# Kernel tuning notes

Hardware: AMD Instinct MI355X
Metric: run time of the kernel (lower is better)

The kernel has to match this reference:

```python
import jax, jax.numpy as jnp
import numpy as np

D = 1024
H = 16
B = 4
S = 2048
NEG = -1000000000.0


def setup_inputs() -> dict:
    key = jax.random.key(0)
    ks = jax.random.split(key, 12)
    s = 0.02
    inp = {
        "Q": jax.random.normal(ks[0], (B, S, D), jnp.float32),
        "K": jax.random.normal(ks[1], (B, S, D), jnp.float32),
        "V": jax.random.normal(ks[2], (B, S, D), jnp.float32),
        # causal mask, broadcastable to [B, H, S, S]
        "mask": jnp.broadcast_to(jnp.tril(jnp.ones((S, S), bool)), (B, 1, S, S)),
        "Wq": jax.random.normal(ks[3], (D, D), jnp.float32) * s,
        "bq": jnp.zeros((D,), jnp.float32),
        "Wk": jax.random.normal(ks[4], (D, D), jnp.float32) * s,
        "bk": jnp.zeros((D,), jnp.float32),
        "Wv": jax.random.normal(ks[5], (D, D), jnp.float32) * s,
        "bv": jnp.zeros((D,), jnp.float32),
        "Wo": jax.random.normal(ks[6], (D, D), jnp.float32) * s,
        "bo": jnp.zeros((D,), jnp.float32),
    }
    return inp


def reference(Q, K, V, mask, Wq, bq, Wk, bk, Wv, bv, Wo, bo):
    d = D // H  # head dim
    def split(x):  # [B,S,D] -> [B,H,S,d]
        Bx, Sx, _ = x.shape
        return x.reshape(Bx, Sx, H, d).transpose(0, 2, 1, 3)

    q = split(Q @ Wq + bq)
    k = split(K @ Wk + bk)
    v = split(V @ Wv + bv)

    scores = jnp.einsum("bhsd,bhtd->bhst", q, k) / jnp.sqrt(jnp.float32(d))
    scores = jnp.where(mask, scores, NEG)
    attn = jax.nn.softmax(scores, axis=-1)
    out = jnp.einsum("bhst,bhtd->bhsd", attn, v)  # [B,H,S,d]
    out = out.transpose(0, 2, 1, 3).reshape(Q.shape[0], Q.shape[1], D)
    return out @ Wo + bo
```

## Files before the change

kernel.cpp:

```cpp
#include <hip/hip_runtime.h>
#include <hip/hip_bf16.h>
#include <type_traits>

#define DEV __device__ __forceinline__

typedef short bf16x8 __attribute__((ext_vector_type(8)));
typedef float f32x4 __attribute__((ext_vector_type(4)));
typedef float f32x16 __attribute__((ext_vector_type(16)));
typedef unsigned u32x4 __attribute__((ext_vector_type(4)));

static DEV unsigned short f2bf(float f) {
  unsigned u = __builtin_bit_cast(unsigned, f);
  u += 0x7FFFu + ((u >> 16) & 1u);
  return (unsigned short)(u >> 16);
}

static DEV unsigned cvtpk(float lo, float hi) {
  unsigned d;
  asm("v_cvt_pk_bf16_f32 %0, %1, %2" : "=v"(d) : "v"(lo), "v"(hi));
  return d;
}

static DEV void pl32(unsigned& x, unsigned& y) {
  asm("v_permlane32_swap_b32 %0, %1" : "+v"(x), "+v"(y));
}

static DEV void gl_lds16(const void* g, void* l) {
  __builtin_amdgcn_global_load_lds(
      (const __attribute__((address_space(1))) unsigned*)g,
      (__attribute__((address_space(3))) unsigned*)l, 16, 0, 0);
}

#define QSCALE 0.18033688f

__global__ __launch_bounds__(256) void wtrans4(const float* __restrict__ W0,
                                               const float* __restrict__ W1,
                                               const float* __restrict__ W2,
                                               const float* __restrict__ W3,
                                               unsigned short* __restrict__ T0,
                                               unsigned short* __restrict__ T1,
                                               unsigned short* __restrict__ T2,
                                               unsigned short* __restrict__ T3) {
  const int z = blockIdx.z;
  const float* W = z == 0 ? W0 : z == 1 ? W1 : z == 2 ? W2 : W3;
  unsigned short* Wt = z == 0 ? T0 : z == 1 ? T1 : z == 2 ? T2 : T3;
  const float wsc = (z == 0) ? QSCALE : 1.0f;
  __shared__ __align__(16) unsigned short T[64][72];
  const int tid = threadIdx.x;
  const int k0 = blockIdx.x * 64, n0 = blockIdx.y * 64;
  const int r = tid >> 4, c4 = (tid & 15) * 4;
  for (int j = 0; j < 4; ++j) {
    int row = j * 16 + r;
    float4 v = *(const float4*)&W[(size_t)(k0 + row) * 1024 + n0 + c4];
    ushort4 w;
    w.x = f2bf(v.x * wsc); w.y = f2bf(v.y * wsc);
    w.z = f2bf(v.z * wsc); w.w = f2bf(v.w * wsc);
    *(ushort4*)&T[row][c4] = w;
  }
  __syncthreads();
  for (int j = 0; j < 4; ++j) {
    int n = j * 16 + r;
    ushort4 w;
    w.x = T[c4 + 0][n]; w.y = T[c4 + 1][n]; w.z = T[c4 + 2][n]; w.w = T[c4 + 3][n];
    *(ushort4*)&Wt[(size_t)(n0 + n) * 1024 + k0 + c4] = w;
  }
}

template <typename InT, typename OutT, bool TRANSV>
DEV void gemm_lds_body(unsigned short* SMG, const InT* __restrict__ X,
                       const unsigned short* __restrict__ Wt,
                       const float* __restrict__ bias, OutT* __restrict__ Y,
                       float bsc) {
  constexpr bool AF32 = std::is_same_v<InT, float>;
  constexpr int HBUF = 24576;
  const int tid = threadIdx.x, lane = tid & 63, wid = tid >> 6;
  const int id = blockIdx.y * 32 + blockIdx.x;
  const int xcd = id & 7, jj = id >> 3;
  const int m0 = (xcd * 4 + (jj & 3)) * 256;
  const int n0 = (jj >> 2) * 128;
  const int wm = (wid >> 1) * 64, wn = (wid & 1) * 64;
  f32x4 acc[4][4] = {};

  const int srowA = tid >> 3;
  const int slotA = ((tid & 7) ^ (srowA & 7)) * 8;
  const int rB = wid * 16 + (lane >> 3);
  const int scolB = (((lane & 7) ^ ((lane >> 3) & 7))) * 8;
  const unsigned short* gB = &Wt[(size_t)(n0 + rB) * 1024 + scolB];
  const unsigned short* gAb = nullptr;
  const float* gAf = nullptr;
  float4 aF[8];

#define ABUF(P) (SMG + (P)*HBUF)
#define BBUF(P) (SMG + (P)*HBUF + 16384)
#define DSWRITE_A(P)                                                              \
  do {                                                                            \
    _Pragma("unroll") for (int q = 0; q < 4; ++q) {                               \
      uint4 w;                                                                    \
      w.x = cvtpk(aF[2 * q].x, aF[2 * q].y);                                      \
      w.y = cvtpk(aF[2 * q].z, aF[2 * q].w);                                      \
      w.z = cvtpk(aF[2 * q + 1].x, aF[2 * q + 1].y);                              \
      w.w = cvtpk(aF[2 * q + 1].z, aF[2 * q + 1].w);                              \
      *(uint4*)&ABUF(P)[(srowA + q * 64) * 64 + slotA] = w;                       \
    }                                                                             \
  } while (0)
#define LOAD_AF(K0)                                                               \
  do {                                                                            \
    _Pragma("unroll") for (int q = 0; q < 4; ++q) {                               \
      aF[2 * q] = *(const float4*)(gAf + (size_t)q * 65536 + (K0));               \
      aF[2 * q + 1] = *(const float4*)(gAf + (size_t)q * 65536 + (K0) + 4);       \
    }                                                                             \
  } while (0)
#define STAGE_B(P, K0)                                                            \
  do {                                                                            \
    _Pragma("unroll") for (int q = 0; q < 2; ++q)                                 \
        gl_lds16(gB + (size_t)q * 8 * 1024 + (K0),                                \
                 &BBUF(P)[(wid * 16 + q * 8) * 64]);                              \
  } while (0)
#define STAGE_AB16(P, K0)                                                         \
  do {                                                                            \
    _Pragma("unroll") for (int q = 0; q < 4; ++q)                                 \
        gl_lds16(gAb + (size_t)q * 8 * 1024 + (K0),                               \
                 &ABUF(P)[(wid * 32 + q * 8) * 64]);                              \
  } while (0)

  if constexpr (AF32) {
    gAf = &X[(size_t)(m0 + srowA) * 1024 + (tid & 7) * 8];
    LOAD_AF(0);
    DSWRITE_A(0);
    LOAD_AF(64);
  } else {
    gAb = &X[(size_t)(m0 + wid * 32 + (lane >> 3)) * 1024 + scolB];
    STAGE_AB16(0, 0);
  }
  STAGE_B(0, 0);
  __syncthreads();

  for (int t = 0; t < 16; ++t) {
    const int p = t & 1;
    if (t + 1 < 16) {
      const int kn = (t + 1) * 64;
      STAGE_B(p ^ 1, kn);
      if constexpr (AF32) {
        DSWRITE_A(p ^ 1);
      } else {
        STAGE_AB16(p ^ 1, kn);
      }
    }
    __builtin_amdgcn_sched_barrier(0);
    if constexpr (AF32) {
      if (t + 2 < 16) LOAD_AF((t + 2) * 64);
    }
    const unsigned short* Asp = ABUF(p);
    const unsigned short* Bsp = BBUF(p);
#pragma unroll
    for (int kk = 0; kk < 2; ++kk) {
      const int kb = ((kk * 4 + (lane >> 4)) ^ (lane & 7)) * 8;
      bf16x8 af[4], bfr[4];
#pragma unroll
      for (int i = 0; i < 4; ++i)
        af[i] = *(const bf16x8*)&Asp[(wm + i * 16 + (lane & 15)) * 64 + kb];
#pragma unroll
      for (int i = 0; i < 4; ++i)
        bfr[i] = *(const bf16x8*)&Bsp[(wn + i * 16 + (lane & 15)) * 64 + kb];
      __builtin_amdgcn_s_setprio(1);
#pragma unroll
      for (int mi = 0; mi < 4; ++mi)
#pragma unroll
        for (int ni = 0; ni < 4; ++ni)
          acc[mi][ni] =
              __builtin_amdgcn_mfma_f32_16x16x32_bf16(af[mi], bfr[ni], acc[mi][ni], 0, 0, 0);
      __builtin_amdgcn_s_setprio(0);
    }
    __syncthreads();
  }
#undef LOAD_AF
#undef DSWRITE_A
#undef STAGE_B
#undef STAGE_AB16
#undef ABUF
#undef BBUF

  if constexpr (TRANSV) {
    const int bt = m0 >> 11;
    const int s0 = m0 & 2047;
    const int h0 = n0 >> 6;
    unsigned short* Tl = SMG;
#pragma unroll
    for (int cch = 0; cch < 4; ++cch) {
      __syncthreads();
      if ((wid >> 1) == cch) {
#pragma unroll
        for (int ni = 0; ni < 4; ++ni) {
          const int n = wn + ni * 16 + (lane & 15);
          const float bv = bias[n0 + n] * bsc;
#pragma unroll
          for (int mi = 0; mi < 4; ++mi) {
            const int mloc = mi * 16 + (lane >> 4) * 4;
#pragma unroll
            for (int r = 0; r < 4; r += 2) {
              const unsigned pk = cvtpk(acc[mi][ni][r] + bv, acc[mi][ni][r + 1] + bv);
              *(unsigned*)&Tl[n * 72 + mloc + r] = pk;
            }
          }
        }
      }
      __syncthreads();
      const int m8 = (tid & 7) * 8;
#pragma unroll
      for (int it = 0; it < 2; ++it) {
        const int nr = (tid >> 3) + it * 64;
        const int h = h0 + (nr >> 6), dv = nr & 63;
        uint4 v = *(const uint4*)&Tl[nr * 72 + m8];
        *(uint4*)&((unsigned short*)Y)[(((size_t)bt * 16 + h) * 64 + dv) * 2048 +
                                       s0 + cch * 64 + m8] = v;
      }
    }
  } else {
    for (int ni = 0; ni < 4; ++ni) {
      const int col = n0 + wn + ni * 16 + (lane & 15);
      const float bv = bias[col] * bsc;
      for (int mi = 0; mi < 4; ++mi) {
        const int row = m0 + wm + mi * 16 + (lane >> 4) * 4;
        for (int r = 0; r < 4; ++r) {
          float v = acc[mi][ni][r] + bv;
          if constexpr (std::is_same_v<OutT, float>)
            Y[(size_t)(row + r) * 1024 + col] = v;
          else
            Y[(size_t)(row + r) * 1024 + col] = f2bf(v);
        }
      }
    }
  }
}

__global__ __launch_bounds__(512) void gemm_qkv3(
    const float* __restrict__ X0, const float* __restrict__ X1,
    const float* __restrict__ X2, const unsigned short* __restrict__ W0,
    const unsigned short* __restrict__ W1, const unsigned short* __restrict__ W2,
    const float* __restrict__ b0, const float* __restrict__ b1,
    const float* __restrict__ b2, unsigned short* __restrict__ Y0,
    unsigned short* __restrict__ Y1, unsigned short* __restrict__ Y2) {
  __shared__ __align__(16) unsigned short SMG[49152];
  const int z = blockIdx.z;
  const float* X = z == 0 ? X0 : z == 1 ? X1 : X2;
  const unsigned short* Wt = z == 0 ? W0 : z == 1 ? W1 : W2;
  const float* bias = z == 0 ? b0 : z == 1 ? b1 : b2;
  unsigned short* Y = z == 0 ? Y0 : z == 1 ? Y1 : Y2;
  if (z == 2)
    gemm_lds_body<float, unsigned short, true>(SMG, X, Wt, bias, Y, 1.0f);
  else
    gemm_lds_body<float, unsigned short, false>(SMG, X, Wt, bias, Y,
                                                z == 0 ? QSCALE : 1.0f);
}

__global__ __launch_bounds__(512) void gemm_out(const unsigned short* __restrict__ X,
                                                const unsigned short* __restrict__ Wt,
                                                const float* __restrict__ bias,
                                                float* __restrict__ Y) {
  __shared__ __align__(16) unsigned short SMG[49152];
  gemm_lds_body<unsigned short, float, false>(SMG, X, Wt, bias, Y, 1.0f);
}

__global__ __launch_bounds__(256) void attn_fwd(const unsigned short* __restrict__ Qb,
                                                const unsigned short* __restrict__ Kb,
                                                const unsigned short* __restrict__ Vt,
                                                unsigned short* __restrict__ Ob) {
  constexpr int KP = 72;
  __shared__ __align__(16) unsigned short SM[4 * 64 * KP];
  const int tid = threadIdx.x, lane = tid & 63, wid = tid >> 6;
  const int l31 = lane & 31, hi = lane >> 5;
  const int id = blockIdx.x;
  const int xcd = id & 7, idx = id >> 3;
  const int bh = xcd + 8 * (idx & 7);
  const int qb = idx >> 3;
  const int q0 = (15 - qb) * 128;
  const int b = bh >> 4, h = bh & 15;
  const size_t rowbase = (size_t)b * 2048;
  const int col0 = h * 64;
  const int qmin = q0 + wid * 32;
  const int myq = qmin + l31;
  const unsigned short* Vrow = Vt + (size_t)bh * 64 * 2048;
  const int rr = tid >> 3, c8 = (tid & 7) * 8;

  bf16x8 qf[4];
#pragma unroll
  for (int c = 0; c < 4; ++c)
    qf[c] = *(const bf16x8*)&Qb[(rowbase + myq) * 1024 + col0 + c * 16 + hi * 8];

  const bf16x8 onesv =
      __builtin_bit_cast(bf16x8, (u32x4){0x3F803F80u, 0x3F803F80u, 0x3F803F80u, 0x3F803F80u});

  f32x16 o[2], rsa;
  o[0] = 0.f; o[1] = 0.f; rsa = 0.f;

  const int NT = q0 / 64 + 2;
  uint4 kr0, kr1, vr0, vr1;
#define LOADT(KV0)                                                              \
  do {                                                                          \
    const int _k = (KV0);                                                       \
    kr0 = *(const uint4*)&Kb[(rowbase + _k + rr) * 1024 + col0 + c8];           \
    kr1 = *(const uint4*)&Kb[(rowbase + _k + rr + 32) * 1024 + col0 + c8];      \
    vr0 = *(const uint4*)&Vrow[(size_t)rr * 2048 + _k + c8];                    \
    vr1 = *(const uint4*)&Vrow[(size_t)(rr + 32) * 2048 + _k + c8];             \
  } while (0)

  LOADT(0);
  {
    unsigned short* Ks = SM;
    unsigned short* Vs = SM + 64 * KP;
    *(uint4*)&Ks[rr * KP + c8] = kr0;
    *(uint4*)&Ks[(rr + 32) * KP + c8] = kr1;
    *(uint4*)&Vs[rr * KP + c8] = vr0;
    *(uint4*)&Vs[(rr + 32) * KP + c8] = vr1;
    LOADT(64);
    __syncthreads();
  }

  for (int t = 0; t < NT; ++t) {
    const int kv0 = t * 64;
    const int p = t & 1;
    if (kv0 <= qmin + 31) {
      const unsigned short* Ks = SM + p * 128 * KP;
      const unsigned short* Vs = Ks + 64 * KP;

      f32x16 s2[2];
      s2[0] = 0.f; s2[1] = 0.f;
      __builtin_amdgcn_s_setprio(1);
#pragma unroll
      for (int m = 0; m < 2; ++m)
#pragma unroll
        for (int c = 0; c < 4; ++c) {
          bf16x8 kf = *(const bf16x8*)&Ks[(m * 32 + l31) * KP + c * 16 + hi * 8];
          s2[m] = __builtin_amdgcn_mfma_f32_32x32x16_bf16(kf, qf[c], s2[m], 0, 0, 0);
        }
      __builtin_amdgcn_s_setprio(0);

      if (kv0 + 63 > qmin) {
        const int thr = l31 + (qmin - kv0);
#pragma unroll
        for (int m = 0; m < 2; ++m)
#pragma unroll
          for (int r = 0; r < 16; ++r) {
            const int kvl = m * 32 + (r & 3) + 8 * (r >> 2) + 4 * hi;
            if (kvl > thr) s2[m][r] = -1.0e30f;
          }
      }

#pragma unroll
      for (int m = 0; m < 2; ++m)
#pragma unroll
        for (int r = 0; r < 16; ++r)
          s2[m][r] = __builtin_amdgcn_exp2f(s2[m][r]);

      bf16x8 pf[4];
#pragma unroll
      for (int m = 0; m < 2; ++m) {
        unsigned a0 = cvtpk(s2[m][0], s2[m][1]), a1 = cvtpk(s2[m][2], s2[m][3]);
        unsigned b0 = cvtpk(s2[m][4], s2[m][5]), b1 = cvtpk(s2[m][6], s2[m][7]);
        pl32(a0, b0);
        pl32(a1, b1);
        pf[2 * m] = __builtin_bit_cast(bf16x8, (u32x4){a0, a1, b0, b1});
        unsigned c0 = cvtpk(s2[m][8], s2[m][9]), c1 = cvtpk(s2[m][10], s2[m][11]);
        unsigned d0 = cvtpk(s2[m][12], s2[m][13]), d1 = cvtpk(s2[m][14], s2[m][15]);
        pl32(c0, d0);
        pl32(c1, d1);
        pf[2 * m + 1] = __builtin_bit_cast(bf16x8, (u32x4){c0, c1, d0, d1});
      }

      __builtin_amdgcn_s_setprio(1);
#pragma unroll
      for (int nt = 0; nt < 2; ++nt)
#pragma unroll
        for (int cc = 0; cc < 4; ++cc) {
          bf16x8 vf = *(const bf16x8*)&Vs[(nt * 32 + l31) * KP + cc * 16 + hi * 8];
          o[nt] = __builtin_amdgcn_mfma_f32_32x32x16_bf16(vf, pf[cc], o[nt], 0, 0, 0);
        }
#pragma unroll
      for (int cc = 0; cc < 4; ++cc)
        rsa = __builtin_amdgcn_mfma_f32_32x32x16_bf16(onesv, pf[cc], rsa, 0, 0, 0);
      __builtin_amdgcn_s_setprio(0);
    }
    if (t + 1 < NT) {
      unsigned short* Ks = SM + (p ^ 1) * 128 * KP;
      unsigned short* Vs = Ks + 64 * KP;
      *(uint4*)&Ks[rr * KP + c8] = kr0;
      *(uint4*)&Ks[(rr + 32) * KP + c8] = kr1;
      *(uint4*)&Vs[rr * KP + c8] = vr0;
      *(uint4*)&Vs[(rr + 32) * KP + c8] = vr1;
      if (t + 2 < NT) LOADT(kv0 + 128);
    }
    __syncthreads();
  }
#undef LOADT

  unsigned short* Os = SM + wid * 32 * KP;
  const float inv = 1.0f / rsa[0];
#pragma unroll
  for (int nt = 0; nt < 2; ++nt)
#pragma unroll
    for (int rq = 0; rq < 4; ++rq)
#pragma unroll
      for (int j = 0; j < 2; ++j) {
        const int r = rq * 4 + 2 * j;
        const unsigned pk = cvtpk(o[nt][r] * inv, o[nt][r + 1] * inv);
        *(unsigned*)&Os[l31 * KP + nt * 32 + 8 * rq + 4 * hi + 2 * j] = pk;
      }
  __syncthreads();
#pragma unroll
  for (int i = 0; i < 4; ++i) {
    const int qq = (lane >> 3) + i * 8;
    const int dvc = (lane & 7) * 8;
    uint4 val = *(const uint4*)&Os[qq * KP + dvc];
    *(uint4*)&Ob[(rowbase + qmin + qq) * 1024 + col0 + dvc] = val;
  }
}

extern "C" void kernel_launch(void* const* d_in, const int* in_sizes, int n_in,
                              void* d_out, int out_size, void* d_ws, size_t ws_size,
                              hipStream_t stream) {
  const float* Q  = (const float*)d_in[0];
  const float* K  = (const float*)d_in[1];
  const float* V  = (const float*)d_in[2];
  const float* Wq = (const float*)d_in[4];
  const float* bq = (const float*)d_in[5];
  const float* Wk = (const float*)d_in[6];
  const float* bk = (const float*)d_in[7];
  const float* Wv = (const float*)d_in[8];
  const float* bv = (const float*)d_in[9];
  const float* Wo = (const float*)d_in[10];
  const float* bo = (const float*)d_in[11];
  float* out = (float*)d_out;

  const size_t MB = 1024 * 1024;
  char* ws = (char*)d_ws;
  unsigned short* qb  = (unsigned short*)(ws + 0 * MB);
  unsigned short* kb  = (unsigned short*)(ws + 16 * MB);
  unsigned short* vtB = (unsigned short*)(ws + 32 * MB);
  unsigned short* ob  = (unsigned short*)(ws + 48 * MB);
  unsigned short* wtq = (unsigned short*)(ws + 64 * MB);
  unsigned short* wtk = (unsigned short*)(ws + 66 * MB);
  unsigned short* wtv = (unsigned short*)(ws + 68 * MB);
  unsigned short* wto = (unsigned short*)(ws + 70 * MB);

  wtrans4<<<dim3(16, 16, 4), 256, 0, stream>>>(Wq, Wk, Wv, Wo, wtq, wtk, wtv, wto);

  gemm_qkv3<<<dim3(32, 8, 3), 512, 0, stream>>>(Q, K, V, wtq, wtk, wtv,
                                                bq, bk, bv, qb, kb, vtB);

  attn_fwd<<<1024, 256, 0, stream>>>(qb, kb, vtB, ob);

  gemm_out<<<dim3(32, 8), 512, 0, stream>>>(ob, wto, bo, out);
}
```

Before: 165.3 us.

## Triple-buffer B tiles in GEMM and replace syncthreads with counted waitcnt barriers

The weight (B) tile staging in the shared GEMM body moves from double to triple buffering, so B loads are issued two k-steps ahead. The LDS layout is split into separate A and B regions, and LDS grows to 112 KB. Full __syncthreads at the end of each step become s_barrier preceded by partial vmcnt waits, which lets in-flight global loads stay outstanding across iterations. The aim is to hide more global-load latency behind MFMA work. The cost is that the hard-coded vmcnt counts must exactly match the number of issued loads, and the larger LDS footprint could reduce occupancy.

```diff
diff --git a/kernel.cpp b/kernel.cpp
--- a/kernel.cpp
+++ b/kernel.cpp
@@ -72,7 +72,6 @@
                        const float* __restrict__ bias, OutT* __restrict__ Y,
                        float bsc) {
   constexpr bool AF32 = std::is_same_v<InT, float>;
-  constexpr int HBUF = 24576;
   const int tid = threadIdx.x, lane = tid & 63, wid = tid >> 6;
   const int id = blockIdx.y * 32 + blockIdx.x;
   const int xcd = id & 7, jj = id >> 3;
@@ -90,8 +89,8 @@
   const float* gAf = nullptr;
   float4 aF[8];
 
-#define ABUF(P) (SMG + (P)*HBUF)
-#define BBUF(P) (SMG + (P)*HBUF + 16384)
+#define ABUF(P) (SMG + (P)*16384)
+#define BBUF(P) (SMG + 32768 + (P)*8192)
 #define DSWRITE_A(P)                                                              \
   do {                                                                            \
     _Pragma("unroll") for (int q = 0; q < 4; ++q) {                               \
@@ -125,33 +124,36 @@
 
   if constexpr (AF32) {
     gAf = &X[(size_t)(m0 + srowA) * 1024 + (tid & 7) * 8];
+    STAGE_B(0, 0);
+    STAGE_B(1, 64);
     LOAD_AF(0);
     DSWRITE_A(0);
     LOAD_AF(64);
+    asm volatile("s_waitcnt vmcnt(8) lgkmcnt(0)" ::: "memory");
   } else {
     gAb = &X[(size_t)(m0 + wid * 32 + (lane >> 3)) * 1024 + scolB];
     STAGE_AB16(0, 0);
-  }
-  STAGE_B(0, 0);
-  __syncthreads();
+    STAGE_B(0, 0);
+    STAGE_B(1, 64);
+    asm volatile("s_waitcnt vmcnt(2) lgkmcnt(0)" ::: "memory");
+  }
+  __builtin_amdgcn_s_barrier();
+  asm volatile("" ::: "memory");
 
   for (int t = 0; t < 16; ++t) {
     const int p = t & 1;
-    if (t + 1 < 16) {
-      const int kn = (t + 1) * 64;
-      STAGE_B(p ^ 1, kn);
-      if constexpr (AF32) {
-        DSWRITE_A(p ^ 1);
-      } else {
-        STAGE_AB16(p ^ 1, kn);
-      }
-    }
-    __builtin_amdgcn_sched_barrier(0);
+    const int bp = t % 3;
     if constexpr (AF32) {
+      if (t + 2 < 16) STAGE_B((t + 2) % 3, (t + 2) * 64);
+      if (t + 1 < 16) DSWRITE_A(p ^ 1);
+      __builtin_amdgcn_sched_barrier(0);
       if (t + 2 < 16) LOAD_AF((t + 2) * 64);
+    } else {
+      if (t + 1 < 16) STAGE_AB16(p ^ 1, (t + 1) * 64);
+      if (t + 2 < 16) STAGE_B((t + 2) % 3, (t + 2) * 64);
     }
     const unsigned short* Asp = ABUF(p);
-    const unsigned short* Bsp = BBUF(p);
+    const unsigned short* Bsp = BBUF(bp);
 #pragma unroll
     for (int kk = 0; kk < 2; ++kk) {
       const int kb = ((kk * 4 + (lane >> 4)) ^ (lane & 7)) * 8;
@@ -171,7 +173,16 @@
               __builtin_amdgcn_mfma_f32_16x16x32_bf16(af[mi], bfr[ni], acc[mi][ni], 0, 0, 0);
       __builtin_amdgcn_s_setprio(0);
     }
-    __syncthreads();
+    if (t + 2 < 16) {
+      if constexpr (AF32)
+        asm volatile("s_waitcnt vmcnt(10) lgkmcnt(0)" ::: "memory");
+      else
+        asm volatile("s_waitcnt vmcnt(2) lgkmcnt(0)" ::: "memory");
+    } else {
+      asm volatile("s_waitcnt vmcnt(0) lgkmcnt(0)" ::: "memory");
+    }
+    __builtin_amdgcn_s_barrier();
+    asm volatile("" ::: "memory");
   }
 #undef LOAD_AF
 #undef DSWRITE_A
@@ -240,7 +251,7 @@
     const float* __restrict__ b0, const float* __restrict__ b1,
     const float* __restrict__ b2, unsigned short* __restrict__ Y0,
     unsigned short* __restrict__ Y1, unsigned short* __restrict__ Y2) {
-  __shared__ __align__(16) unsigned short SMG[49152];
+  __shared__ __align__(16) unsigned short SMG[57344];
   const int z = blockIdx.z;
   const float* X = z == 0 ? X0 : z == 1 ? X1 : X2;
   const unsigned short* Wt = z == 0 ? W0 : z == 1 ? W1 : W2;
@@ -257,7 +268,7 @@
                                                 const unsigned short* __restrict__ Wt,
                                                 const float* __restrict__ bias,
                                                 float* __restrict__ Y) {
-  __shared__ __align__(16) unsigned short SMG[49152];
+  __shared__ __align__(16) unsigned short SMG[57344];
   gemm_lds_body<unsigned short, float, false>(SMG, X, Wt, bias, Y, 1.0f);
 }
 
```

Measured after the change: 165.6 us. No clear change (+0.2%).
